# Performance work log

Measured on AMD Instinct MI355X. Metric: run time of the kernel, lower is better.

Reference implementation:

```python
import jax, jax.numpy as jnp
import numpy as np

INPUT_SIZE = 128
OUTPUT_SIZE = 128
HIDDEN = 8
BATCH = 1024
N = INPUT_SIZE * OUTPUT_SIZE  # number of tiny subnetworks


def setup_inputs() -> dict:
    key = jax.random.key(0)
    ks = jax.random.split(key, 7)
    s = 0.5  # modest init scale
    return {
        "x": jax.random.normal(ks[0], (BATCH, INPUT_SIZE), dtype=jnp.float32),
        "W1": jax.random.normal(ks[1], (N, HIDDEN, 1), dtype=jnp.float32) * s,
        "b1": jax.random.normal(ks[2], (N, HIDDEN), dtype=jnp.float32) * s,
        "W2": jax.random.normal(ks[3], (N, HIDDEN, HIDDEN), dtype=jnp.float32) * s,
        "b2": jax.random.normal(ks[4], (N, HIDDEN), dtype=jnp.float32) * s,
        "W3": jax.random.normal(ks[5], (N, 1, HIDDEN), dtype=jnp.float32) * s,
        "b3": jax.random.normal(ks[6], (N, 1), dtype=jnp.float32) * s,
    }


def reference(x, W1, b1, W2, b2, W3, b3):
    # x: [B, input_size]. Subnet n = i*output_size + o consumes feature i.
    B = x.shape[0]
    # x.T repeat_interleave(output_size, dim=0).unsqueeze(-1) -> [N, B, 1]
    xe = jnp.repeat(x.T, OUTPUT_SIZE, axis=0)[:, :, None]
    # torch Linear: y = x @ W.T + b, batched over subnet dim n
    h = jax.nn.relu(jnp.einsum('nbi,nhi->nbh', xe, W1) + b1[:, None, :])
    h = jax.nn.relu(jnp.einsum('nbi,nhi->nbh', h, W2) + b2[:, None, :])
    o = jnp.einsum('nbh,noh->nbo', h, W3) + b3[:, None, :]  # [N, B, 1]
    o = o[..., 0].reshape(INPUT_SIZE, OUTPUT_SIZE, B)
    return o.sum(axis=0).T  # [B, output_size]
```

## Files before the change

kernel.cpp:

```cpp
#include <hip/hip_runtime.h>

#define INPUT_SIZE 128
#define OUTPUT_SIZE 128
#define HIDDEN 8
#define BATCH 1024

#define ICH 16
#define IPC (INPUT_SIZE / ICH)
#define TPB 128
#define BPT 8

typedef __fp16 half2v __attribute__((ext_vector_type(2)));

#if defined(__has_builtin)
#if __has_builtin(__builtin_amdgcn_fdot2)
#define HAS_FDOT2 1
#endif
#endif
#ifndef HAS_FDOT2
#define HAS_FDOT2 0
#endif

__global__ void prep_kernel(const float* __restrict__ x,
                            const float* __restrict__ W2,
                            float* __restrict__ xT,
                            __fp16* __restrict__ W2h) {
    if (blockIdx.x < 128) {
        __shared__ float tile[32][33];
        const int bx = blockIdx.x;
        const int i0 = (bx & 3) * 32;
        const int b0 = (bx >> 2) * 32;
        const int tx = threadIdx.x & 31;
        const int ty = threadIdx.x >> 5;
#pragma unroll
        for (int r = ty; r < 32; r += 8)
            tile[r][tx] = x[(b0 + r) * INPUT_SIZE + (i0 + tx)];
        __syncthreads();
#pragma unroll
        for (int r = ty; r < 32; r += 8)
            xT[(i0 + r) * BATCH + (b0 + tx)] = tile[tx][r];
    } else {
        const size_t idx = (size_t)(blockIdx.x - 128) * 256 + threadIdx.x;
        const float4 v = *(const float4*)(W2 + 4 * idx);
        const half2v a = __builtin_amdgcn_cvt_pkrtz(v.x, v.y);
        const half2v b = __builtin_amdgcn_cvt_pkrtz(v.z, v.w);
        float2 st;
        st.x = __builtin_bit_cast(float, a);
        st.y = __builtin_bit_cast(float, b);
        *(float2*)(W2h + 4 * idx) = st;
    }
}

__global__ void zero_out_kernel(float* __restrict__ out, int n) {
    int idx = blockIdx.x * blockDim.x + threadIdx.x;
    if (idx < n) out[idx] = 0.0f;
}

template <bool PARTIALS>
__global__ __launch_bounds__(TPB, 3)
void mlpkan_kernel(const float* __restrict__ xT,
                   const float* __restrict__ W1, const float* __restrict__ b1,
                   const __fp16* __restrict__ W2h, const float* __restrict__ b2,
                   const float* __restrict__ W3, const float* __restrict__ b3,
                   float* __restrict__ partials, float* __restrict__ out) {
    const int o   = blockIdx.x;
    const int ic  = blockIdx.y;
    const int tid = threadIdx.x;

    float acc[BPT];
#pragma unroll
    for (int j = 0; j < BPT; ++j) acc[j] = 0.0f;

#pragma unroll 1
    for (int ii = 0; ii < IPC; ++ii) {
        const int i = ic * IPC + ii;
        const int n = i * OUTPUT_SIZE + o;

        float s[BPT];
#pragma unroll
        for (int j = 0; j < BPT; ++j)
            s[j] = xT[(size_t)i * BATCH + tid + j * TPB];

        const float4 w1a = *(const float4*)(W1 + (size_t)n * 8);
        const float4 w1b = *(const float4*)(W1 + (size_t)n * 8 + 4);
        const float4 b1a = *(const float4*)(b1 + (size_t)n * 8);
        const float4 b1b = *(const float4*)(b1 + (size_t)n * 8 + 4);
        const float4 b2a = *(const float4*)(b2 + (size_t)n * 8);
        const float4 b2b = *(const float4*)(b2 + (size_t)n * 8 + 4);
        const float4 w3a = *(const float4*)(W3 + (size_t)n * 8);
        const float4 w3b = *(const float4*)(W3 + (size_t)n * 8 + 4);
        const float  bb3 = b3[n];

        half2v w2p[8][4];
#pragma unroll
        for (int h = 0; h < 8; ++h) {
            const float4 row = *(const float4*)((const char*)W2h + (size_t)n * 128 + h * 16);
            w2p[h][0] = __builtin_bit_cast(half2v, row.x);
            w2p[h][1] = __builtin_bit_cast(half2v, row.y);
            w2p[h][2] = __builtin_bit_cast(half2v, row.z);
            w2p[h][3] = __builtin_bit_cast(half2v, row.w);
        }

        const float w1r[8] = {w1a.x, w1a.y, w1a.z, w1a.w, w1b.x, w1b.y, w1b.z, w1b.w};
        const float b1r[8] = {b1a.x, b1a.y, b1a.z, b1a.w, b1b.x, b1b.y, b1b.z, b1b.w};
        const float b2r[8] = {b2a.x, b2a.y, b2a.z, b2a.w, b2b.x, b2b.y, b2b.z, b2b.w};
        const float w3r[8] = {w3a.x, w3a.y, w3a.z, w3a.w, w3b.x, w3b.y, w3b.z, w3b.w};

#pragma unroll
        for (int j = 0; j < BPT; ++j) {
            const float sj = s[j];
            float h1[8];
#pragma unroll
            for (int k = 0; k < 8; ++k)
                h1[k] = fmaxf(fmaf(w1r[k], sj, b1r[k]), 0.0f);

#if HAS_FDOT2
            half2v hp[4];
#pragma unroll
            for (int q = 0; q < 4; ++q)
                hp[q] = __builtin_amdgcn_cvt_pkrtz(h1[2 * q], h1[2 * q + 1]);

            float h2[8];
#pragma unroll
            for (int h = 0; h < 8; ++h) {
                float v = b2r[h];
#pragma unroll
                for (int q = 0; q < 4; ++q)
                    v = __builtin_amdgcn_fdot2(w2p[h][q], hp[q], v, false);
                h2[h] = fmaxf(v, 0.0f);
            }
#else
            float h2[8];
#pragma unroll
            for (int h = 0; h < 8; ++h) {
                float v = b2r[h];
#pragma unroll
                for (int q = 0; q < 4; ++q) {
                    v = fmaf((float)w2p[h][q][0], h1[2 * q], v);
                    v = fmaf((float)w2p[h][q][1], h1[2 * q + 1], v);
                }
                h2[h] = fmaxf(v, 0.0f);
            }
#endif
            float v3 = bb3;
#pragma unroll
            for (int k = 0; k < 8; ++k)
                v3 = fmaf(w3r[k], h2[k], v3);
            acc[j] += v3;
        }
    }

    if (PARTIALS) {
#pragma unroll
        for (int j = 0; j < BPT; ++j)
            partials[((size_t)ic * OUTPUT_SIZE + o) * BATCH + tid + j * TPB] = acc[j];
    } else {
#pragma unroll
        for (int j = 0; j < BPT; ++j)
            atomicAdd(&out[(size_t)(tid + j * TPB) * OUTPUT_SIZE + o], acc[j]);
    }
}

__global__ void reduce_kernel(const float* __restrict__ partials,
                              float* __restrict__ out) {
    __shared__ float tile[32][33];
    const int o0 = blockIdx.x * 32;
    const int b0 = blockIdx.y * 32;
    const int tx = threadIdx.x;
    const int ty = threadIdx.y;
#pragma unroll
    for (int r = ty; r < 32; r += 16) {
        float v = 0.0f;
#pragma unroll
        for (int icc = 0; icc < ICH; ++icc)
            v += partials[((size_t)icc * OUTPUT_SIZE + o0 + r) * BATCH + b0 + tx];
        tile[r][tx] = v;
    }
    __syncthreads();
#pragma unroll
    for (int r = ty; r < 32; r += 16)
        out[(size_t)(b0 + r) * OUTPUT_SIZE + o0 + tx] = tile[tx][r];
}

extern "C" void kernel_launch(void* const* d_in, const int* in_sizes, int n_in,
                              void* d_out, int out_size, void* d_ws, size_t ws_size,
                              hipStream_t stream) {
    const float* x  = (const float*)d_in[0];
    const float* W1 = (const float*)d_in[1];
    const float* b1 = (const float*)d_in[2];
    const float* W2 = (const float*)d_in[3];
    const float* b2 = (const float*)d_in[4];
    const float* W3 = (const float*)d_in[5];
    const float* b3 = (const float*)d_in[6];
    float* out = (float*)d_out;

    const size_t xt_elems   = (size_t)INPUT_SIZE * BATCH;
    const size_t part_elems = (size_t)ICH * OUTPUT_SIZE * BATCH;
    const size_t w2h_bytes  = (size_t)16384 * 64 * sizeof(__fp16);
    const size_t need_bytes = (xt_elems + part_elems) * sizeof(float) + w2h_bytes;

    dim3 mgrid(OUTPUT_SIZE, ICH);

    if (ws_size >= need_bytes) {
        float*   xT       = (float*)d_ws;
        float*   partials = xT + xt_elems;
        __fp16*  W2h      = (__fp16*)(partials + part_elems);

        prep_kernel<<<1152, 256, 0, stream>>>(x, W2, xT, W2h);
        mlpkan_kernel<true><<<mgrid, TPB, 0, stream>>>(xT, W1, b1, W2h, b2, W3, b3,
                                                       partials, out);
        dim3 rgrid(OUTPUT_SIZE / 32, BATCH / 32);
        reduce_kernel<<<rgrid, dim3(32, 16), 0, stream>>>(partials, out);
    } else {
        const int nz = BATCH * OUTPUT_SIZE;
        zero_out_kernel<<<(nz + 255) / 256, 256, 0, stream>>>(out, nz);
        if (ws_size >= xt_elems * sizeof(float) + w2h_bytes) {
            float*  xT  = (float*)d_ws;
            __fp16* W2h = (__fp16*)(xT + xt_elems);
            prep_kernel<<<1152, 256, 0, stream>>>(x, W2, xT, W2h);
            mlpkan_kernel<false><<<mgrid, TPB, 0, stream>>>(xT, W1, b1, W2h, b2, W3, b3,
                                                            nullptr, out);
        }
    }
}
```

Baseline: 111.2 us.

## Stage per-subnet weights in LDS, vectorize x loads, restructure MLP loop

All weights and biases for the block's 8 subnets are loaded once, cooperatively, into shared memory at kernel start. The per-iteration weight reads then come from LDS instead of scattered global loads. The layer-1 outputs for all 8 batch elements are computed and packed to fp16 first, then W2 is loaded and layer 2 runs, which is meant to lower live registers so launch bounds can rise from 3 to 4 waves per SIMD. The x loads and partial stores now use float4 with a remapped batch index per thread. This adds a __syncthreads and LDS traffic, and may cause register spills at the higher occupancy target.

```diff
diff --git a/kernel.cpp b/kernel.cpp
--- a/kernel.cpp
+++ b/kernel.cpp
@@ -9,6 +9,7 @@
 #define IPC (INPUT_SIZE / ICH)
 #define TPB 128
 #define BPT 8
+#define SLOT 68
 
 typedef __fp16 half2v __attribute__((ext_vector_type(2)));
 
@@ -57,16 +58,41 @@
 }
 
 template <bool PARTIALS>
-__global__ __launch_bounds__(TPB, 3)
+__global__ __launch_bounds__(TPB, 4)
 void mlpkan_kernel(const float* __restrict__ xT,
                    const float* __restrict__ W1, const float* __restrict__ b1,
                    const __fp16* __restrict__ W2h, const float* __restrict__ b2,
                    const float* __restrict__ W3, const float* __restrict__ b3,
                    float* __restrict__ partials, float* __restrict__ out) {
+    __shared__ float wlds[IPC * SLOT];
+
     const int o   = blockIdx.x;
     const int ic  = blockIdx.y;
     const int tid = threadIdx.x;
 
+    {
+        const int ii  = tid >> 4;
+        const int idx = tid & 15;
+        const int n   = (ic * IPC + ii) * OUTPUT_SIZE + o;
+        float4 v;
+        int dst;
+        if (idx < 2) {
+            v = *(const float4*)(W1 + (size_t)n * 8 + idx * 4);          dst = 0  + idx * 4;
+        } else if (idx < 4) {
+            v = *(const float4*)(b1 + (size_t)n * 8 + (idx - 2) * 4);    dst = 8  + (idx - 2) * 4;
+        } else if (idx < 6) {
+            v = *(const float4*)(b2 + (size_t)n * 8 + (idx - 4) * 4);    dst = 16 + (idx - 4) * 4;
+        } else if (idx < 8) {
+            v = *(const float4*)(W3 + (size_t)n * 8 + (idx - 6) * 4);    dst = 24 + (idx - 6) * 4;
+        } else {
+            v = *(const float4*)((const char*)W2h + (size_t)n * 128 + (idx - 8) * 16);
+            dst = 36 + (idx - 8) * 4;
+        }
+        *(float4*)&wlds[ii * SLOT + dst] = v;
+        if (idx == 0) wlds[ii * SLOT + 32] = b3[n];
+    }
+    __syncthreads();
+
     float acc[BPT];
 #pragma unroll
     for (int j = 0; j < BPT; ++j) acc[j] = 0.0f;
@@ -74,38 +100,20 @@
 #pragma unroll 1
     for (int ii = 0; ii < IPC; ++ii) {
         const int i = ic * IPC + ii;
-        const int n = i * OUTPUT_SIZE + o;
-
-        float s[BPT];
-#pragma unroll
-        for (int j = 0; j < BPT; ++j)
-            s[j] = xT[(size_t)i * BATCH + tid + j * TPB];
-
-        const float4 w1a = *(const float4*)(W1 + (size_t)n * 8);
-        const float4 w1b = *(const float4*)(W1 + (size_t)n * 8 + 4);
-        const float4 b1a = *(const float4*)(b1 + (size_t)n * 8);
-        const float4 b1b = *(const float4*)(b1 + (size_t)n * 8 + 4);
-        const float4 b2a = *(const float4*)(b2 + (size_t)n * 8);
-        const float4 b2b = *(const float4*)(b2 + (size_t)n * 8 + 4);
-        const float4 w3a = *(const float4*)(W3 + (size_t)n * 8);
-        const float4 w3b = *(const float4*)(W3 + (size_t)n * 8 + 4);
-        const float  bb3 = b3[n];
-
-        half2v w2p[8][4];
-#pragma unroll
-        for (int h = 0; h < 8; ++h) {
-            const float4 row = *(const float4*)((const char*)W2h + (size_t)n * 128 + h * 16);
-            w2p[h][0] = __builtin_bit_cast(half2v, row.x);
-            w2p[h][1] = __builtin_bit_cast(half2v, row.y);
-            w2p[h][2] = __builtin_bit_cast(half2v, row.z);
-            w2p[h][3] = __builtin_bit_cast(half2v, row.w);
-        }
-
+        const float* w = &wlds[ii * SLOT];
+
+        const float4 sA = *(const float4*)(xT + (size_t)i * BATCH + 4 * tid);
+        const float4 sB = *(const float4*)(xT + (size_t)i * BATCH + 512 + 4 * tid);
+        const float s[BPT] = {sA.x, sA.y, sA.z, sA.w, sB.x, sB.y, sB.z, sB.w};
+
+        const float4 w1a = *(const float4*)(w + 0);
+        const float4 w1b = *(const float4*)(w + 4);
+        const float4 b1a = *(const float4*)(w + 8);
+        const float4 b1b = *(const float4*)(w + 12);
         const float w1r[8] = {w1a.x, w1a.y, w1a.z, w1a.w, w1b.x, w1b.y, w1b.z, w1b.w};
         const float b1r[8] = {b1a.x, b1a.y, b1a.z, b1a.w, b1b.x, b1b.y, b1b.z, b1b.w};
-        const float b2r[8] = {b2a.x, b2a.y, b2a.z, b2a.w, b2b.x, b2b.y, b2b.z, b2b.w};
-        const float w3r[8] = {w3a.x, w3a.y, w3a.z, w3a.w, w3b.x, w3b.y, w3b.z, w3b.w};
-
+
+        half2v h1p[BPT][4];
 #pragma unroll
         for (int j = 0; j < BPT; ++j) {
             const float sj = s[j];
@@ -113,36 +121,54 @@
 #pragma unroll
             for (int k = 0; k < 8; ++k)
                 h1[k] = fmaxf(fmaf(w1r[k], sj, b1r[k]), 0.0f);
-
+#pragma unroll
+            for (int q = 0; q < 4; ++q)
+                h1p[j][q] = __builtin_amdgcn_cvt_pkrtz(h1[2 * q], h1[2 * q + 1]);
+        }
+
+        const float4 b2a = *(const float4*)(w + 16);
+        const float4 b2b = *(const float4*)(w + 20);
+        const float4 w3a = *(const float4*)(w + 24);
+        const float4 w3b = *(const float4*)(w + 28);
+        const float  b3r = w[32];
+        const float b2r[8] = {b2a.x, b2a.y, b2a.z, b2a.w, b2b.x, b2b.y, b2b.z, b2b.w};
+        const float w3r[8] = {w3a.x, w3a.y, w3a.z, w3a.w, w3b.x, w3b.y, w3b.z, w3b.w};
+
+        half2v w2p[8][4];
+#pragma unroll
+        for (int r = 0; r < 8; ++r) {
+            const float4 row = *(const float4*)(w + 36 + 4 * r);
+            w2p[r][0] = __builtin_bit_cast(half2v, row.x);
+            w2p[r][1] = __builtin_bit_cast(half2v, row.y);
+            w2p[r][2] = __builtin_bit_cast(half2v, row.z);
+            w2p[r][3] = __builtin_bit_cast(half2v, row.w);
+        }
+
+#pragma unroll
+        for (int j = 0; j < BPT; ++j) {
+            float h2[8];
 #if HAS_FDOT2
-            half2v hp[4];
-#pragma unroll
-            for (int q = 0; q < 4; ++q)
-                hp[q] = __builtin_amdgcn_cvt_pkrtz(h1[2 * q], h1[2 * q + 1]);
-
-            float h2[8];
 #pragma unroll
             for (int h = 0; h < 8; ++h) {
                 float v = b2r[h];
 #pragma unroll
                 for (int q = 0; q < 4; ++q)
-                    v = __builtin_amdgcn_fdot2(w2p[h][q], hp[q], v, false);
+                    v = __builtin_amdgcn_fdot2(w2p[h][q], h1p[j][q], v, false);
                 h2[h] = fmaxf(v, 0.0f);
             }
 #else
-            float h2[8];
 #pragma unroll
             for (int h = 0; h < 8; ++h) {
                 float v = b2r[h];
 #pragma unroll
                 for (int q = 0; q < 4; ++q) {
-                    v = fmaf((float)w2p[h][q][0], h1[2 * q], v);
-                    v = fmaf((float)w2p[h][q][1], h1[2 * q + 1], v);
+                    v = fmaf((float)w2p[h][q][0], (float)h1p[j][q][0], v);
+                    v = fmaf((float)w2p[h][q][1], (float)h1p[j][q][1], v);
                 }
                 h2[h] = fmaxf(v, 0.0f);
             }
 #endif
-            float v3 = bb3;
+            float v3 = b3r;
 #pragma unroll
             for (int k = 0; k < 8; ++k)
                 v3 = fmaf(w3r[k], h2[k], v3);
@@ -151,13 +177,17 @@
     }
 
     if (PARTIALS) {
-#pragma unroll
-        for (int j = 0; j < BPT; ++j)
-            partials[((size_t)ic * OUTPUT_SIZE + o) * BATCH + tid + j * TPB] = acc[j];
+        float* base = partials + ((size_t)ic * OUTPUT_SIZE + o) * BATCH;
+        float4 pa = {acc[0], acc[1], acc[2], acc[3]};
+        float4 pb = {acc[4], acc[5], acc[6], acc[7]};
+        *(float4*)(base + 4 * tid)       = pa;
+        *(float4*)(base + 512 + 4 * tid) = pb;
     } else {
 #pragma unroll
-        for (int j = 0; j < BPT; ++j)
-            atomicAdd(&out[(size_t)(tid + j * TPB) * OUTPUT_SIZE + o], acc[j]);
+        for (int j = 0; j < BPT; ++j) {
+            const int b = (j < 4) ? (4 * tid + j) : (512 + 4 * tid + (j - 4));
+            atomicAdd(&out[(size_t)b * OUTPUT_SIZE + o], acc[j]);
+        }
     }
 }
 
```

Result: no change. 110.7 us (-0.4%).
